# Kernel optimization log

Hardware: AMD Instinct MI355X
Metric: run time of the kernel (lower is better)

Reference implementation:

```python
import jax, jax.numpy as jnp
import numpy as np

D_MODEL = 1024

def setup_inputs() -> dict:
    key = jax.random.key(0)
    kx, kq, kk, kv, ko = jax.random.split(key, 5)
    x = jax.random.normal(kx, (4, 4096, D_MODEL), dtype=jnp.float32)
    w_q = jax.random.normal(kq, (D_MODEL, D_MODEL), dtype=jnp.float32)
    w_k = jax.random.normal(kk, (D_MODEL, D_MODEL), dtype=jnp.float32)
    w_v = jax.random.normal(kv, (D_MODEL, D_MODEL), dtype=jnp.float32)
    w_o = jax.random.normal(ko, (D_MODEL, D_MODEL), dtype=jnp.float32)
    return {"x": x, "w_q": w_q, "w_k": w_k, "w_v": w_v, "w_o": w_o}

def reference(x, w_q, w_k, w_v, w_o):
    # Q/K/V projections: [B,T,D] @ [D,D] -> [B,T,D]
    q = jnp.einsum('btd,de->bte', x, w_q)
    k = jnp.einsum('btd,de->bte', x, w_k)
    v = jnp.einsum('btd,de->bte', x, w_v)
    # Unnormalized attention: scores [B,T,T] (no softmax)
    scores = jnp.einsum('btd,bsd->bts', q, k)
    attn_output = jnp.einsum('bts,bsd->btd', scores, v)
    # Output projection
    output = jnp.einsum('btd,de->bte', attn_output, w_o)
    return output
```

## Files before the change

### kernel.cpp

```cpp
#include <hip/hip_runtime.h>
#include <hip/hip_bf16.h>
#include <stdint.h>

typedef unsigned short u16;
typedef short bf16x8 __attribute__((ext_vector_type(8)));
typedef float f32x4 __attribute__((ext_vector_type(4)));

#define GLOAD16(gp, lp) __builtin_amdgcn_global_load_lds( \
    (const __attribute__((address_space(1))) uint32_t*)(gp), \
    (__attribute__((address_space(3))) uint32_t*)(lp), 16, 0, 0)

#define VMCNT10 do { asm volatile("s_waitcnt vmcnt(10)" ::: "memory"); \
                     __builtin_amdgcn_sched_barrier(0); } while (0)
#define SBAR    do { __builtin_amdgcn_s_barrier(); \
                     __builtin_amdgcn_sched_barrier(0); } while (0)
#define LGKM0   do { asm volatile("s_waitcnt lgkmcnt(0)" ::: "memory"); \
                     __builtin_amdgcn_sched_barrier(0); } while (0)

__device__ __forceinline__ u16 f2bf(float f) {
  union { float f; uint32_t u; } x; x.f = f;
  return (u16)((x.u + 0x7FFFu + ((x.u >> 16) & 1u)) >> 16);
}
__device__ __forceinline__ float bf2f(u16 h) {
  union { uint32_t u; float f; } x; x.u = (uint32_t)h << 16;
  return x.f;
}

__device__ __forceinline__ void xcd_swizzle(int& bx, int& by, int& bz) {
  const int gx = gridDim.x, gy = gridDim.y;
  const int nwg = gx * gy * (int)gridDim.z;
  const int lin = ((int)blockIdx.z * gy + (int)blockIdx.y) * gx + (int)blockIdx.x;
  const int q = nwg >> 3;
  const int wl = (lin & 7) * q + (lin >> 3);
  bz = wl / (gx * gy);
  const int rem = wl - bz * gx * gy;
  by = rem / gx;
  bx = rem - by * gx;
}

__global__ __launch_bounds__(256) void cast_all(const float* __restrict__ x,
                                                const float* __restrict__ wq,
                                                const float* __restrict__ wk,
                                                const float* __restrict__ wv,
                                                const float* __restrict__ wo,
                                                u16* __restrict__ xb,
                                                u16* __restrict__ xT,
                                                u16* __restrict__ WA,
                                                u16* __restrict__ WBb) {
  __shared__ u16 ldsT[64][264];
  const int lin = blockIdx.x;
  const int t = threadIdx.x;
  if (lin < 1024) {
    const int dt = lin >> 6;
    const int tt = lin & 63;
    const int d0 = dt * 64, t0 = tt * 256;
    const int lr = t >> 2, lc = (t & 3) * 16;
#pragma unroll
    for (int i = 0; i < 4; ++i) {
      const int row = t0 + i * 64 + lr;
      const float* src = x + (size_t)row * 1024 + d0 + lc;
      u16 pl[16];
#pragma unroll
      for (int j = 0; j < 4; ++j) {
        float4 v = *(const float4*)&src[j * 4];
        pl[j * 4 + 0] = f2bf(v.x); pl[j * 4 + 1] = f2bf(v.y);
        pl[j * 4 + 2] = f2bf(v.z); pl[j * 4 + 3] = f2bf(v.w);
      }
      u16* pdst = xb + (size_t)row * 1024 + d0 + lc;
      *(uint4*)&pdst[0] = *(const uint4*)&pl[0];
      *(uint4*)&pdst[8] = *(const uint4*)&pl[8];
#pragma unroll
      for (int j = 0; j < 16; ++j) ldsT[lc + j][i * 64 + lr] = pl[j];
    }
    __syncthreads();
    const int dl = t >> 2, seg = (t & 3) * 64;
    u16* dst = xT + (size_t)(d0 + dl) * 16384 + t0 + seg;
    const u16* srcl = &ldsT[dl][seg];
#pragma unroll
    for (int k = 0; k < 8; ++k)
      *(uint4*)&dst[k * 8] = *(const uint4*)&srcl[k * 8];
  } else {
    const int w = lin - 1024;
    const int z = w >> 8, tl = w & 255;
    const int r0 = (tl >> 4) * 64, c0 = (tl & 15) * 64;
    const float* in = z == 0 ? wq : z == 1 ? wk : z == 2 ? wv : wo;
    u16* o = z == 0 ? WA : z == 1 ? WBb : z == 2 ? WBb + 1048576 : WA + 1048576;
    const int lr = t >> 2, lc = (t & 3) * 16;
    const float* src = in + (size_t)(r0 + lr) * 1024 + c0 + lc;
    if (z < 3) {
      u16 p[16];
#pragma unroll
      for (int j = 0; j < 4; ++j) {
        float4 v = *(const float4*)&src[j * 4];
        p[j * 4 + 0] = f2bf(v.x); p[j * 4 + 1] = f2bf(v.y);
        p[j * 4 + 2] = f2bf(v.z); p[j * 4 + 3] = f2bf(v.w);
      }
      u16* dst = o + (size_t)(r0 + lr) * 1024 + c0 + lc;
      *(uint4*)&dst[0] = *(const uint4*)&p[0];
      *(uint4*)&dst[8] = *(const uint4*)&p[8];
    } else {
      float (*tile)[65] = (float(*)[65])ldsT;
#pragma unroll
      for (int j = 0; j < 4; ++j) {
        float4 v = *(const float4*)&src[j * 4];
        tile[lr][lc + j * 4 + 0] = v.x;
        tile[lr][lc + j * 4 + 1] = v.y;
        tile[lr][lc + j * 4 + 2] = v.z;
        tile[lr][lc + j * 4 + 3] = v.w;
      }
      __syncthreads();
      u16 tr[16];
#pragma unroll
      for (int j = 0; j < 16; ++j) tr[j] = f2bf(tile[lc + j][lr]);
      u16* dst = o + (size_t)(c0 + lr) * 1024 + r0 + lc;
      *(uint4*)&dst[0] = *(const uint4*)&tr[0];
      *(uint4*)&dst[8] = *(const uint4*)&tr[8];
    }
  }
}

__global__ __launch_bounds__(512) void gram_w12(const u16* __restrict__ xT,
                                                u16* __restrict__ Gp,
                                                const u16* __restrict__ WA,
                                                const u16* __restrict__ WBb,
                                                u16* __restrict__ W12) {
  __shared__ u16 lds[2 * 8192];
  const int lin = blockIdx.x;
  const int wl = (lin & 7) * 88 + (lin >> 3);
  const u16 *A, *B;
  u16* Cb;
  int lda, ldc;
  if (wl < 576) {
    const int z = wl / 36, t5 = wl - z * 36;
    const int b = z >> 2, kc = z & 3;
    int ti = 0;
    while ((ti + 1) * (ti + 2) / 2 <= t5) ++ti;
    const int tj = t5 - ti * (ti + 1) / 2;
    const u16* Ap = xT + (size_t)b * 4096 + (size_t)kc * 1024;
    A = Ap + (size_t)(ti * 128) * 16384;
    B = Ap + (size_t)(tj * 128) * 16384;
    lda = 16384;
    Cb = Gp + ((size_t)z * 36 + t5) * 16384;
    ldc = 128;
  } else {
    const int w = wl - 576;
    const int z2 = w >> 6, tl = w & 63;
    const int by = tl >> 3, bx = tl & 7;
    A = WA + (size_t)z2 * 1048576 + (size_t)(by * 128) * 1024;
    B = WBb + (size_t)z2 * 1048576 + (size_t)(bx * 128) * 1024;
    lda = 1024;
    Cb = W12 + (size_t)z2 * 1048576 + (size_t)(by * 128) * 1024 + bx * 128;
    ldc = 1024;
  }

  const int t = threadIdx.x;
  const int l = t & 63;
  const int wid = t >> 6;
  const int wr = wid >> 2, wc = wid & 3;
  const int lr16 = l & 15, hi = l >> 4;

  f32x4 acc[4][2];
#pragma unroll
  for (int m = 0; m < 4; ++m)
#pragma unroll
    for (int n = 0; n < 2; ++n) acc[m][n] = (f32x4){0.f, 0.f, 0.f, 0.f};

  for (int kt = 0; kt < 1024; kt += 64) {
    __syncthreads();
#pragma unroll
    for (int i = 0; i < 2; ++i) {
      int s = i * 512 + t;
      int row = s >> 3, cp = s & 7;
      int clog = cp ^ (row & 7);
      GLOAD16(A + (size_t)row * lda + kt + clog * 8, &lds[s * 8]);
    }
#pragma unroll
    for (int i = 0; i < 2; ++i) {
      int s = i * 512 + t;
      int row = s >> 3, cp = s & 7;
      int clog = cp ^ (row & 7);
      GLOAD16(B + (size_t)row * lda + kt + clog * 8, &lds[8192 + s * 8]);
    }
    asm volatile("s_waitcnt vmcnt(0)" ::: "memory");
    __syncthreads();
#pragma unroll
    for (int ks = 0; ks < 2; ++ks) {
      bf16x8 af[4], bfr[2];
#pragma unroll
      for (int m = 0; m < 4; ++m) {
        int row = wr * 64 + m * 16 + lr16;
        int p = (ks * 4 + hi) ^ (row & 7);
        af[m] = *(const bf16x8*)&lds[row * 64 + p * 8];
      }
#pragma unroll
      for (int n = 0; n < 2; ++n) {
        int row = wc * 32 + n * 16 + lr16;
        int p = (ks * 4 + hi) ^ (row & 7);
        bfr[n] = *(const bf16x8*)&lds[8192 + row * 64 + p * 8];
      }
#pragma unroll
      for (int m = 0; m < 4; ++m)
#pragma unroll
        for (int n = 0; n < 2; ++n)
          acc[m][n] = __builtin_amdgcn_mfma_f32_16x16x32_bf16(af[m], bfr[n], acc[m][n], 0, 0, 0);
    }
  }

#pragma unroll
  for (int m = 0; m < 4; ++m) {
    int row0 = wr * 64 + m * 16 + hi * 4;
#pragma unroll
    for (int n = 0; n < 2; ++n) {
      int col = wc * 32 + n * 16 + lr16;
      f32x4 v = acc[m][n];
#pragma unroll
      for (int r = 0; r < 4; ++r) Cb[(size_t)(row0 + r) * ldc + col] = f2bf(v[r]);
    }
  }
}

__global__ __launch_bounds__(512) void gemm_bt8(const u16* __restrict__ A,
                                                const u16* __restrict__ B,
                                                u16* __restrict__ C,
                                                int lda, int ldb, int ldc, int K,
                                                size_t sA, size_t sB, size_t sC) {
  __shared__ u16 lds[2 * 8192];
  int bx, by, bz;
  xcd_swizzle(bx, by, bz);
  A += (size_t)bz * sA;
  B += (size_t)bz * sB;
  const int t = threadIdx.x;
  const int l = t & 63;
  const int wid = t >> 6;
  const int wr = wid >> 2, wc = wid & 3;
  const int lr16 = l & 15, hi = l >> 4;
  const int mBase = by * 128;
  const int nBase = bx * 128;

  f32x4 acc[4][2];
#pragma unroll
  for (int m = 0; m < 4; ++m)
#pragma unroll
    for (int n = 0; n < 2; ++n) acc[m][n] = (f32x4){0.f, 0.f, 0.f, 0.f};

  for (int kt = 0; kt < K; kt += 64) {
    __syncthreads();
#pragma unroll
    for (int i = 0; i < 2; ++i) {
      int s = i * 512 + t;
      int row = s >> 3, cp = s & 7;
      int clog = cp ^ (row & 7);
      GLOAD16(A + (size_t)(mBase + row) * lda + kt + clog * 8, &lds[s * 8]);
    }
#pragma unroll
    for (int i = 0; i < 2; ++i) {
      int s = i * 512 + t;
      int row = s >> 3, cp = s & 7;
      int clog = cp ^ (row & 7);
      GLOAD16(B + (size_t)(nBase + row) * ldb + kt + clog * 8, &lds[8192 + s * 8]);
    }
    asm volatile("s_waitcnt vmcnt(0)" ::: "memory");
    __syncthreads();
#pragma unroll
    for (int ks = 0; ks < 2; ++ks) {
      bf16x8 af[4], bfr[2];
#pragma unroll
      for (int m = 0; m < 4; ++m) {
        int row = wr * 64 + m * 16 + lr16;
        int p = (ks * 4 + hi) ^ (row & 7);
        af[m] = *(const bf16x8*)&lds[row * 64 + p * 8];
      }
#pragma unroll
      for (int n = 0; n < 2; ++n) {
        int row = wc * 32 + n * 16 + lr16;
        int p = (ks * 4 + hi) ^ (row & 7);
        bfr[n] = *(const bf16x8*)&lds[8192 + row * 64 + p * 8];
      }
#pragma unroll
      for (int m = 0; m < 4; ++m)
#pragma unroll
        for (int n = 0; n < 2; ++n)
          acc[m][n] = __builtin_amdgcn_mfma_f32_16x16x32_bf16(af[m], bfr[n], acc[m][n], 0, 0, 0);
    }
  }

#pragma unroll
  for (int m = 0; m < 4; ++m) {
    int row0 = mBase + wr * 64 + m * 16 + hi * 4;
#pragma unroll
    for (int n = 0; n < 2; ++n) {
      int col = nBase + wc * 32 + n * 16 + lr16;
      f32x4 v = acc[m][n];
      u16* Cb = C + (size_t)bz * sC;
#pragma unroll
      for (int r = 0; r < 4; ++r) Cb[(size_t)(row0 + r) * ldc + col] = f2bf(v[r]);
    }
  }
}

__global__ __launch_bounds__(256) void reduce_mirror(const u16* __restrict__ Gp,
                                                     u16* __restrict__ G) {
  __shared__ u16 ldsT[128][136];
  const int t5 = blockIdx.x;
  const int b = blockIdx.y;
  int ti = 0;
  while ((ti + 1) * (ti + 2) / 2 <= t5) ++ti;
  const int tj = t5 - ti * (ti + 1) / 2;
  const int tid = threadIdx.x;
  const int rr = tid >> 4, ccc = (tid & 15) * 8;
  u16* Gb = G + (size_t)b * 1048576;
  const size_t ZS = (size_t)36 * 16384;
  const u16* base = Gp + ((size_t)(b * 4) * 36 + t5) * 16384;
#pragma unroll
  for (int i = 0; i < 8; ++i) {
    int row = i * 16 + rr;
    const u16* p = base + row * 128 + ccc;
    u16 a0[8], a1[8], a2[8], a3[8], o[8];
    *(uint4*)a0 = *(const uint4*)&p[0];
    *(uint4*)a1 = *(const uint4*)&p[ZS];
    *(uint4*)a2 = *(const uint4*)&p[2 * ZS];
    *(uint4*)a3 = *(const uint4*)&p[3 * ZS];
#pragma unroll
    for (int j = 0; j < 8; ++j)
      o[j] = f2bf(bf2f(a0[j]) + bf2f(a1[j]) + bf2f(a2[j]) + bf2f(a3[j]));
    *(uint4*)&Gb[(size_t)(ti * 128 + row) * 1024 + tj * 128 + ccc] = *(const uint4*)o;
    *(uint4*)&ldsT[row][ccc] = *(const uint4*)o;
  }
  if (ti != tj) {
    __syncthreads();
#pragma unroll
    for (int i = 0; i < 8; ++i) {
      int row = i * 16 + rr;
      u16 m8[8];
#pragma unroll
      for (int j = 0; j < 8; ++j) m8[j] = ldsT[ccc + j][row];
      *(uint4*)&Gb[(size_t)(tj * 128 + row) * 1024 + ti * 128 + ccc] = *(const uint4*)m8;
    }
  }
}

template <bool F32OUT>
__device__ __forceinline__ void gemm256_core(const u16* __restrict__ A,
                                             const u16* __restrict__ B,
                                             void* __restrict__ C,
                                             int lda, int ldb, int ldc, int K,
                                             int mBase, int nBase, u16* lds) {
  const int t = threadIdx.x;
  const int l = t & 63;
  const int wid = t >> 6;
  const int wr = wid >> 2;
  const int wc = wid & 3;
  const int lr16 = l & 15, hi = l >> 4;
  const int rl0 = t >> 3;
  const int rl1 = rl0 + 64;
  const int cp  = t & 7;
  const int cs  = cp ^ (rl0 & 7);
  const int NT = K >> 6;

  f32x4 acc[8][4];
#pragma unroll
  for (int m = 0; m < 8; ++m)
#pragma unroll
    for (int n = 0; n < 4; ++n) acc[m][n] = (f32x4){0.f, 0.f, 0.f, 0.f};

  auto stage = [&](const u16* g0, int ld, u16* d) {
    GLOAD16(g0 + (size_t)rl0 * ld + cs * 8, d + rl0 * 64 + cp * 8);
    GLOAD16(g0 + (size_t)rl1 * ld + cs * 8, d + rl1 * 64 + cp * 8);
  };
  stage(A + (size_t)mBase * lda,          lda, lds + 0);
  stage(B + (size_t)nBase * ldb,          ldb, lds + 16384);
  stage(B + (size_t)(nBase + 128) * ldb,  ldb, lds + 24576);
  stage(A + (size_t)(mBase + 128) * lda,  lda, lds + 8192);
  stage(B + (size_t)nBase * ldb + 64,         ldb, lds + 32768 + 16384);
  stage(A + (size_t)mBase * lda + 64,         lda, lds + 32768);
  stage(B + (size_t)(nBase + 128) * ldb + 64, ldb, lds + 32768 + 24576);

  bf16x8 af[4][2], b0[2][2], b1[2][2];

  for (int tt = 0; tt < NT; ++tt) {
    const int cur = tt & 1;
    u16* bufA = lds + cur * 32768;
    u16* bufB = bufA + 16384;
    u16* bufN = lds + ((tt + 1) & 1) * 32768;
    int t1 = tt + 1; if (t1 >= NT) t1 -= NT;
    int t2 = tt + 2; if (t2 >= NT) t2 -= NT;
    const int k1 = t1 * 64, k2 = t2 * 64;

    VMCNT10;
    SBAR;
    stage(A + (size_t)(mBase + 128) * lda + k1, lda, bufN + 8192);
#pragma unroll
    for (int mi = 0; mi < 4; ++mi) {
      int row = wr * 64 + mi * 16 + lr16;
#pragma unroll
      for (int kk = 0; kk < 2; ++kk) {
        int p = (kk * 4 + hi) ^ (row & 7);
        af[mi][kk] = *(const bf16x8*)&bufA[row * 64 + p * 8];
      }
    }
#pragma unroll
    for (int ni = 0; ni < 2; ++ni) {
      int row = wc * 32 + ni * 16 + lr16;
#pragma unroll
      for (int kk = 0; kk < 2; ++kk) {
        int p = (kk * 4 + hi) ^ (row & 7);
        b0[ni][kk] = *(const bf16x8*)&bufB[row * 64 + p * 8];
      }
    }
    LGKM0;
    __builtin_amdgcn_s_setprio(1);
#pragma unroll
    for (int kk = 0; kk < 2; ++kk)
#pragma unroll
      for (int mi = 0; mi < 4; ++mi)
#pragma unroll
        for (int ni = 0; ni < 2; ++ni)
          acc[mi][ni] = __builtin_amdgcn_mfma_f32_16x16x32_bf16(af[mi][kk], b0[ni][kk], acc[mi][ni], 0, 0, 0);
    __builtin_amdgcn_s_setprio(0);

    VMCNT10;
    SBAR;
    stage(B + (size_t)nBase * ldb + k2, ldb, bufB);
#pragma unroll
    for (int ni = 0; ni < 2; ++ni) {
      int row = 128 + wc * 32 + ni * 16 + lr16;
#pragma unroll
      for (int kk = 0; kk < 2; ++kk) {
        int p = (kk * 4 + hi) ^ (row & 7);
        b1[ni][kk] = *(const bf16x8*)&bufB[row * 64 + p * 8];
      }
    }
    LGKM0;
    __builtin_amdgcn_s_setprio(1);
#pragma unroll
    for (int kk = 0; kk < 2; ++kk)
#pragma unroll
      for (int mi = 0; mi < 4; ++mi)
#pragma unroll
        for (int ni = 0; ni < 2; ++ni)
          acc[mi][2 + ni] = __builtin_amdgcn_mfma_f32_16x16x32_bf16(af[mi][kk], b1[ni][kk], acc[mi][2 + ni], 0, 0, 0);
    __builtin_amdgcn_s_setprio(0);

    VMCNT10;
    SBAR;
    stage(A + (size_t)mBase * lda + k2, lda, bufA);
#pragma unroll
    for (int mi = 0; mi < 4; ++mi) {
      int row = 128 + wr * 64 + mi * 16 + lr16;
#pragma unroll
      for (int kk = 0; kk < 2; ++kk) {
        int p = (kk * 4 + hi) ^ (row & 7);
        af[mi][kk] = *(const bf16x8*)&bufA[row * 64 + p * 8];
      }
    }
    LGKM0;
    __builtin_amdgcn_s_setprio(1);
#pragma unroll
    for (int kk = 0; kk < 2; ++kk)
#pragma unroll
      for (int mi = 0; mi < 4; ++mi)
#pragma unroll
        for (int ni = 0; ni < 2; ++ni)
          acc[4 + mi][2 + ni] = __builtin_amdgcn_mfma_f32_16x16x32_bf16(af[mi][kk], b1[ni][kk], acc[4 + mi][2 + ni], 0, 0, 0);
    __builtin_amdgcn_s_setprio(0);

    SBAR;
    stage(B + (size_t)(nBase + 128) * ldb + k2, ldb, bufB + 8192);
    __builtin_amdgcn_s_setprio(1);
#pragma unroll
    for (int kk = 0; kk < 2; ++kk)
#pragma unroll
      for (int mi = 0; mi < 4; ++mi)
#pragma unroll
        for (int ni = 0; ni < 2; ++ni)
          acc[4 + mi][ni] = __builtin_amdgcn_mfma_f32_16x16x32_bf16(af[mi][kk], b0[ni][kk], acc[4 + mi][ni], 0, 0, 0);
    __builtin_amdgcn_s_setprio(0);
  }

#pragma unroll
  for (int m = 0; m < 8; ++m) {
    int row0 = mBase + (m >> 2) * 128 + wr * 64 + (m & 3) * 16 + hi * 4;
#pragma unroll
    for (int n = 0; n < 4; ++n) {
      int col = nBase + (n >> 1) * 128 + wc * 32 + (n & 1) * 16 + lr16;
      f32x4 v = acc[m][n];
      if (F32OUT) {
        float* Cf = (float*)C;
#pragma unroll
        for (int r = 0; r < 4; ++r) Cf[(size_t)(row0 + r) * ldc + col] = v[r];
      } else {
        u16* Cb = (u16*)C;
#pragma unroll
        for (int r = 0; r < 4; ++r) Cb[(size_t)(row0 + r) * ldc + col] = f2bf(v[r]);
      }
    }
  }
}

__global__ __launch_bounds__(512) void gemm256_out(const u16* __restrict__ xb,
                                                   const u16* __restrict__ PT,
                                                   float* __restrict__ out) {
  __shared__ u16 lds[65536];
  int bx, by, bz;
  xcd_swizzle(bx, by, bz);
  const u16* Bp = PT + (size_t)(by >> 4) * 1048576;
  gemm256_core<true>(xb, Bp, out, 1024, 1024, 1024, 1024, by * 256, bx * 256, lds);
}

extern "C" void kernel_launch(void* const* d_in, const int* in_sizes, int n_in,
                              void* d_out, int out_size, void* d_ws, size_t ws_size,
                              hipStream_t stream) {
  const float* x  = (const float*)d_in[0];
  const float* wq = (const float*)d_in[1];
  const float* wk = (const float*)d_in[2];
  const float* wv = (const float*)d_in[3];
  const float* wo = (const float*)d_in[4];
  float* out = (float*)d_out;

  u16* ws = (u16*)d_ws;
  const size_t MW = 1048576;
  u16* xb  = ws;
  u16* xT  = ws + 16 * MW;
  u16* WA  = ws + 32 * MW;
  u16* WBb = ws + 34 * MW;
  u16* W12 = ws + 36 * MW;
  u16* G   = ws + 38 * MW;
  u16* S   = ws + 42 * MW;
  u16* PT  = ws + 46 * MW;
  u16* Gp  = ws + 50 * MW;

  cast_all<<<2048, 256, 0, stream>>>(x, wq, wk, wv, wo, xb, xT, WA, WBb);

  gram_w12<<<704, 512, 0, stream>>>(xT, Gp, WA, WBb, W12);
  reduce_mirror<<<dim3(36, 4), 256, 0, stream>>>(Gp, G);

  gemm_bt8<<<dim3(8, 8, 4), 512, 0, stream>>>(W12 + MW, G, S,
                                              1024, 1024, 1024, 1024,
                                              0, MW, MW);
  gemm_bt8<<<dim3(8, 8, 4), 512, 0, stream>>>(S, W12, PT,
                                              1024, 1024, 1024, 1024,
                                              MW, 0, MW);
  gemm256_out<<<dim3(4, 64), 512, 0, stream>>>(xb, PT, out);
}
```

Baseline: 156.2 us.

## Split cast into streaming kernel plus separate tiled transpose of x

The fused cast-and-transpose kernel becomes a purely streaming fp32-to-bf16 cast for x and the three row-major weights, with only w_o still transposed through LDS. A new kernel then transposes the bf16 x into contiguous 128x64 tiles, so each K-step of the Gram GEMM reads one contiguous 16 KB block instead of strided rows. The aim is more coalesced cast traffic and better locality for the Gram loads, at the cost of an extra launch and an extra read and write of bf16 x.

```diff
diff --git a/kernel.cpp b/kernel.cpp
--- a/kernel.cpp
+++ b/kernel.cpp
@@ -38,88 +38,90 @@
   bx = rem - by * gx;
 }
 
-__global__ __launch_bounds__(256) void cast_all(const float* __restrict__ x,
-                                                const float* __restrict__ wq,
-                                                const float* __restrict__ wk,
-                                                const float* __restrict__ wv,
-                                                const float* __restrict__ wo,
-                                                u16* __restrict__ xb,
-                                                u16* __restrict__ xT,
-                                                u16* __restrict__ WA,
-                                                u16* __restrict__ WBb) {
-  __shared__ u16 ldsT[64][264];
+__global__ __launch_bounds__(256) void cast_stream(const float* __restrict__ x,
+                                                   const float* __restrict__ wq,
+                                                   const float* __restrict__ wk,
+                                                   const float* __restrict__ wv,
+                                                   const float* __restrict__ wo,
+                                                   u16* __restrict__ xb,
+                                                   u16* __restrict__ WA,
+                                                   u16* __restrict__ WBb) {
+  __shared__ float tile[64][65];
   const int lin = blockIdx.x;
   const int t = threadIdx.x;
-  if (lin < 1024) {
-    const int dt = lin >> 6;
-    const int tt = lin & 63;
-    const int d0 = dt * 64, t0 = tt * 256;
+  if (lin < 2048) {
+    const float* src = x + (size_t)lin * 8192;
+    u16* dst = xb + (size_t)lin * 8192;
+#pragma unroll
+    for (int i = 0; i < 4; ++i) {
+      const int e = i * 2048 + t * 8;
+      float4 a = *(const float4*)&src[e];
+      float4 b = *(const float4*)&src[e + 4];
+      u16 p[8];
+      p[0] = f2bf(a.x); p[1] = f2bf(a.y); p[2] = f2bf(a.z); p[3] = f2bf(a.w);
+      p[4] = f2bf(b.x); p[5] = f2bf(b.y); p[6] = f2bf(b.z); p[7] = f2bf(b.w);
+      *(uint4*)&dst[e] = *(const uint4*)p;
+    }
+  } else if (lin < 3584) {
+    const int e0 = (lin - 2048) * 2048 + t * 8;
+    const int w = e0 >> 20;
+    const int loc = e0 & 1048575;
+    const float* in = w == 0 ? wq : w == 1 ? wk : wv;
+    u16* o = w == 0 ? WA : w == 1 ? WBb : WBb + 1048576;
+    float4 a = *(const float4*)&in[loc];
+    float4 b = *(const float4*)&in[loc + 4];
+    u16 p[8];
+    p[0] = f2bf(a.x); p[1] = f2bf(a.y); p[2] = f2bf(a.z); p[3] = f2bf(a.w);
+    p[4] = f2bf(b.x); p[5] = f2bf(b.y); p[6] = f2bf(b.z); p[7] = f2bf(b.w);
+    *(uint4*)&o[loc] = *(const uint4*)p;
+  } else {
+    const int w2 = lin - 3584;
+    const int r0 = (w2 >> 4) * 64, c0 = (w2 & 15) * 64;
     const int lr = t >> 2, lc = (t & 3) * 16;
-#pragma unroll
-    for (int i = 0; i < 4; ++i) {
-      const int row = t0 + i * 64 + lr;
-      const float* src = x + (size_t)row * 1024 + d0 + lc;
-      u16 pl[16];
-#pragma unroll
-      for (int j = 0; j < 4; ++j) {
-        float4 v = *(const float4*)&src[j * 4];
-        pl[j * 4 + 0] = f2bf(v.x); pl[j * 4 + 1] = f2bf(v.y);
-        pl[j * 4 + 2] = f2bf(v.z); pl[j * 4 + 3] = f2bf(v.w);
-      }
-      u16* pdst = xb + (size_t)row * 1024 + d0 + lc;
-      *(uint4*)&pdst[0] = *(const uint4*)&pl[0];
-      *(uint4*)&pdst[8] = *(const uint4*)&pl[8];
-#pragma unroll
-      for (int j = 0; j < 16; ++j) ldsT[lc + j][i * 64 + lr] = pl[j];
+    const float* src = wo + (size_t)(r0 + lr) * 1024 + c0 + lc;
+#pragma unroll
+    for (int j = 0; j < 4; ++j) {
+      float4 v = *(const float4*)&src[j * 4];
+      tile[lr][lc + j * 4 + 0] = v.x;
+      tile[lr][lc + j * 4 + 1] = v.y;
+      tile[lr][lc + j * 4 + 2] = v.z;
+      tile[lr][lc + j * 4 + 3] = v.w;
     }
     __syncthreads();
-    const int dl = t >> 2, seg = (t & 3) * 64;
-    u16* dst = xT + (size_t)(d0 + dl) * 16384 + t0 + seg;
-    const u16* srcl = &ldsT[dl][seg];
-#pragma unroll
-    for (int k = 0; k < 8; ++k)
-      *(uint4*)&dst[k * 8] = *(const uint4*)&srcl[k * 8];
-  } else {
-    const int w = lin - 1024;
-    const int z = w >> 8, tl = w & 255;
-    const int r0 = (tl >> 4) * 64, c0 = (tl & 15) * 64;
-    const float* in = z == 0 ? wq : z == 1 ? wk : z == 2 ? wv : wo;
-    u16* o = z == 0 ? WA : z == 1 ? WBb : z == 2 ? WBb + 1048576 : WA + 1048576;
-    const int lr = t >> 2, lc = (t & 3) * 16;
-    const float* src = in + (size_t)(r0 + lr) * 1024 + c0 + lc;
-    if (z < 3) {
-      u16 p[16];
-#pragma unroll
-      for (int j = 0; j < 4; ++j) {
-        float4 v = *(const float4*)&src[j * 4];
-        p[j * 4 + 0] = f2bf(v.x); p[j * 4 + 1] = f2bf(v.y);
-        p[j * 4 + 2] = f2bf(v.z); p[j * 4 + 3] = f2bf(v.w);
-      }
-      u16* dst = o + (size_t)(r0 + lr) * 1024 + c0 + lc;
-      *(uint4*)&dst[0] = *(const uint4*)&p[0];
-      *(uint4*)&dst[8] = *(const uint4*)&p[8];
-    } else {
-      float (*tile)[65] = (float(*)[65])ldsT;
-#pragma unroll
-      for (int j = 0; j < 4; ++j) {
-        float4 v = *(const float4*)&src[j * 4];
-        tile[lr][lc + j * 4 + 0] = v.x;
-        tile[lr][lc + j * 4 + 1] = v.y;
-        tile[lr][lc + j * 4 + 2] = v.z;
-        tile[lr][lc + j * 4 + 3] = v.w;
-      }
-      __syncthreads();
-      u16 tr[16];
-#pragma unroll
-      for (int j = 0; j < 16; ++j) tr[j] = f2bf(tile[lc + j][lr]);
-      u16* dst = o + (size_t)(c0 + lr) * 1024 + r0 + lc;
-      *(uint4*)&dst[0] = *(const uint4*)&tr[0];
-      *(uint4*)&dst[8] = *(const uint4*)&tr[8];
-    }
-  }
-}
-
-__global__ __launch_bounds__(512) void gram_w12(const u16* __restrict__ xT,
+    u16 tr[16];
+#pragma unroll
+    for (int j = 0; j < 16; ++j) tr[j] = f2bf(tile[lc + j][lr]);
+    u16* dst = WA + 1048576 + (size_t)(c0 + lr) * 1024 + r0 + lc;
+    *(uint4*)&dst[0] = *(const uint4*)&tr[0];
+    *(uint4*)&dst[8] = *(const uint4*)&tr[8];
+  }
+}
+
+__global__ __launch_bounds__(256) void transpose_x(const u16* __restrict__ xb,
+                                                   u16* __restrict__ xTt) {
+  __shared__ u16 ldsT[128][72];
+  const int tile = blockIdx.x;
+  const int dtile = tile >> 8, tchunk = tile & 255;
+  const int t = threadIdx.x;
+  const int lr = t >> 2;
+  const int dq = (t & 3) * 32;
+  const u16* src = xb + (size_t)(tchunk * 64 + lr) * 1024 + dtile * 128 + dq;
+#pragma unroll
+  for (int i = 0; i < 4; ++i) {
+    u16 v[8];
+    *(uint4*)v = *(const uint4*)&src[i * 8];
+#pragma unroll
+    for (int j = 0; j < 8; ++j) ldsT[dq + i * 8 + j][lr] = v[j];
+  }
+  __syncthreads();
+  const int d = t >> 1, seg = (t & 1) * 32;
+  u16* dst = xTt + (size_t)tile * 8192 + d * 64 + seg;
+#pragma unroll
+  for (int i = 0; i < 4; ++i)
+    *(uint4*)&dst[i * 8] = *(const uint4*)&ldsT[d][seg + i * 8];
+}
+
+__global__ __launch_bounds__(512) void gram_w12(const u16* __restrict__ xTt,
                                                 u16* __restrict__ Gp,
                                                 const u16* __restrict__ WA,
                                                 const u16* __restrict__ WBb,
@@ -127,28 +129,28 @@
   __shared__ u16 lds[2 * 8192];
   const int lin = blockIdx.x;
   const int wl = (lin & 7) * 88 + (lin >> 3);
-  const u16 *A, *B;
+  const u16 *Abase, *Bbase;
   u16* Cb;
-  int lda, ldc;
+  int lda, sKt, ldc;
   if (wl < 576) {
     const int z = wl / 36, t5 = wl - z * 36;
     const int b = z >> 2, kc = z & 3;
     int ti = 0;
     while ((ti + 1) * (ti + 2) / 2 <= t5) ++ti;
     const int tj = t5 - ti * (ti + 1) / 2;
-    const u16* Ap = xT + (size_t)b * 4096 + (size_t)kc * 1024;
-    A = Ap + (size_t)(ti * 128) * 16384;
-    B = Ap + (size_t)(tj * 128) * 16384;
-    lda = 16384;
+    const int tc0 = b * 64 + kc * 16;
+    Abase = xTt + (size_t)(ti * 256 + tc0) * 8192;
+    Bbase = xTt + (size_t)(tj * 256 + tc0) * 8192;
+    lda = 64; sKt = 8192;
     Cb = Gp + ((size_t)z * 36 + t5) * 16384;
     ldc = 128;
   } else {
     const int w = wl - 576;
     const int z2 = w >> 6, tl = w & 63;
     const int by = tl >> 3, bx = tl & 7;
-    A = WA + (size_t)z2 * 1048576 + (size_t)(by * 128) * 1024;
-    B = WBb + (size_t)z2 * 1048576 + (size_t)(bx * 128) * 1024;
-    lda = 1024;
+    Abase = WA + (size_t)z2 * 1048576 + (size_t)(by * 128) * 1024;
+    Bbase = WBb + (size_t)z2 * 1048576 + (size_t)(bx * 128) * 1024;
+    lda = 1024; sKt = 64;
     Cb = W12 + (size_t)z2 * 1048576 + (size_t)(by * 128) * 1024 + bx * 128;
     ldc = 1024;
   }
@@ -165,21 +167,23 @@
 #pragma unroll
     for (int n = 0; n < 2; ++n) acc[m][n] = (f32x4){0.f, 0.f, 0.f, 0.f};
 
-  for (int kt = 0; kt < 1024; kt += 64) {
+  for (int s = 0; s < 16; ++s) {
     __syncthreads();
+    const u16* As = Abase + (size_t)s * sKt;
+    const u16* Bs = Bbase + (size_t)s * sKt;
 #pragma unroll
     for (int i = 0; i < 2; ++i) {
-      int s = i * 512 + t;
-      int row = s >> 3, cp = s & 7;
+      int slot = i * 512 + t;
+      int row = slot >> 3, cp = slot & 7;
       int clog = cp ^ (row & 7);
-      GLOAD16(A + (size_t)row * lda + kt + clog * 8, &lds[s * 8]);
+      GLOAD16(As + (size_t)row * lda + clog * 8, &lds[slot * 8]);
     }
 #pragma unroll
     for (int i = 0; i < 2; ++i) {
-      int s = i * 512 + t;
-      int row = s >> 3, cp = s & 7;
+      int slot = i * 512 + t;
+      int row = slot >> 3, cp = slot & 7;
       int clog = cp ^ (row & 7);
-      GLOAD16(B + (size_t)row * lda + kt + clog * 8, &lds[8192 + s * 8]);
+      GLOAD16(Bs + (size_t)row * lda + clog * 8, &lds[8192 + slot * 8]);
     }
     asm volatile("s_waitcnt vmcnt(0)" ::: "memory");
     __syncthreads();
@@ -520,7 +524,7 @@
   u16* ws = (u16*)d_ws;
   const size_t MW = 1048576;
   u16* xb  = ws;
-  u16* xT  = ws + 16 * MW;
+  u16* xTt = ws + 16 * MW;
   u16* WA  = ws + 32 * MW;
   u16* WBb = ws + 34 * MW;
   u16* W12 = ws + 36 * MW;
@@ -529,9 +533,10 @@
   u16* PT  = ws + 46 * MW;
   u16* Gp  = ws + 50 * MW;
 
-  cast_all<<<2048, 256, 0, stream>>>(x, wq, wk, wv, wo, xb, xT, WA, WBb);
-
-  gram_w12<<<704, 512, 0, stream>>>(xT, Gp, WA, WBb, W12);
+  cast_stream<<<3840, 256, 0, stream>>>(x, wq, wk, wv, wo, xb, WA, WBb);
+  transpose_x<<<2048, 256, 0, stream>>>(xb, xTt);
+
+  gram_w12<<<704, 512, 0, stream>>>(xTt, Gp, WA, WBb, W12);
   reduce_mirror<<<dim3(36, 4), 256, 0, stream>>>(Gp, G);
 
   gemm_bt8<<<dim3(8, 8, 4), 512, 0, stream>>>(W12 + MW, G, S,
```

Result: no change. 156.4 us (+0.1%).
